# Performance work log

Measured on AMD Instinct MI355X. Metric: run time of the kernel, lower is better.

The kernel has to match this reference:

```python
import jax, jax.numpy as jnp
import numpy as np
import math

B, T, H, W = 32, 256, 16, 16
NE, NH, NL = 768, 12, 8
DH = NE // NH
SEQ_LEN = 1024


def _ln(x, g, b, eps=1e-5):
    m = jnp.mean(x, axis=-1, keepdims=True)
    v = jnp.mean((x - m) ** 2, axis=-1, keepdims=True)
    return (x - m) * jax.lax.rsqrt(v + eps) * g + b


def setup_inputs() -> dict:
    key = jax.random.key(0)
    ks = jax.random.split(key, 24)
    s = 0.02
    d = {}
    d["img_feat"] = jax.random.normal(ks[0], (B, 2048, H, W), jnp.float32)
    d["vm_patches"] = jax.random.normal(ks[1], (B, T, 256), jnp.float32)
    d["fm_patches"] = jax.random.normal(ks[2], (B, T, 256), jnp.float32)
    # token embedding params
    d["conv_w"] = jax.random.normal(ks[3], (NE // 2, 2048, 3, 3), jnp.float32) * s
    d["conv_b"] = jnp.zeros((NE // 2,), jnp.float32)
    d["vm_w"] = jax.random.normal(ks[4], (256, NE // 4), jnp.float32) * s
    d["vm_b"] = jnp.zeros((NE // 4,), jnp.float32)
    d["fm_w"] = jax.random.normal(ks[5], (256, NE // 4), jnp.float32) * s
    d["fm_b"] = jnp.zeros((NE // 4,), jnp.float32)
    d["pos_emb"] = jax.random.normal(ks[6], (SEQ_LEN, NE), jnp.float32) * s
    # stacked per-layer block params (leading dim NL, consumed by lax.scan)
    d["ln1_g"] = jnp.ones((NL, NE), jnp.float32)
    d["ln1_b"] = jnp.zeros((NL, NE), jnp.float32)
    d["Wq"] = jax.random.normal(ks[7], (NL, NE, NE), jnp.float32) * s
    d["bq"] = jnp.zeros((NL, NE), jnp.float32)
    d["Wk"] = jax.random.normal(ks[8], (NL, NE, NE), jnp.float32) * s
    d["bk"] = jnp.zeros((NL, NE), jnp.float32)
    d["Wv"] = jax.random.normal(ks[9], (NL, NE, NE), jnp.float32) * s
    d["bv"] = jnp.zeros((NL, NE), jnp.float32)
    d["Wo"] = jax.random.normal(ks[10], (NL, NE, NE), jnp.float32) * s
    d["bo"] = jnp.zeros((NL, NE), jnp.float32)
    d["ln2_g"] = jnp.ones((NL, NE), jnp.float32)
    d["ln2_b"] = jnp.zeros((NL, NE), jnp.float32)
    d["W1"] = jax.random.normal(ks[11], (NL, NE, 4 * NE), jnp.float32) * s
    d["b1"] = jnp.zeros((NL, 4 * NE), jnp.float32)
    d["W2"] = jax.random.normal(ks[12], (NL, 4 * NE, NE), jnp.float32) * s
    d["b2"] = jnp.zeros((NL, NE), jnp.float32)
    # prediction head params
    d["dec_ln1_g"] = jnp.ones((NE,), jnp.float32)
    d["dec_ln1_b"] = jnp.zeros((NE,), jnp.float32)
    d["dec_w"] = jax.random.normal(ks[13], (NE, NE), jnp.float32) * s
    d["dec_b"] = jnp.zeros((NE,), jnp.float32)
    d["dec_ln2_g"] = jnp.ones((NE,), jnp.float32)
    d["dec_ln2_b"] = jnp.zeros((NE,), jnp.float32)
    d["head_w"] = jax.random.normal(ks[14], (NE, 256), jnp.float32) * s
    d["head_b"] = jnp.zeros((256,), jnp.float32)
    return d


def reference(img_feat, vm_patches, fm_patches, conv_w, conv_b, vm_w, vm_b, fm_w, fm_b,
              pos_emb, ln1_g, ln1_b, Wq, bq, Wk, bk, Wv, bv, Wo, bo, ln2_g, ln2_b,
              W1, b1, W2, b2, dec_ln1_g, dec_ln1_b, dec_w, dec_b, dec_ln2_g, dec_ln2_b,
              head_w, head_b):
    # conv token embed: [B,2048,H,W] -> [B, NE//2, H, W] -> [B, T, NE//2]
    i_emb = jax.lax.conv_general_dilated(
        img_feat, conv_w, (1, 1), "SAME",
        dimension_numbers=("NCHW", "OIHW", "NCHW")) + conv_b[None, :, None, None]
    i_emb = i_emb.reshape(B, NE // 2, T).transpose(0, 2, 1)
    vm_emb = vm_patches @ vm_w + vm_b  # [B,T,NE//4]
    fm_emb = fm_patches @ fm_w + fm_b  # [B,T,NE//4]
    x = jnp.concatenate([i_emb, vm_emb, fm_emb], axis=2) + pos_emb[:T][None]  # [B,T,NE]

    scale = 1.0 / math.sqrt(DH)

    def block(x, p):
        g1, bb1_, wq, bq_, wk, bk_, wv, bv_, wo, bo_, g2, bb2_, w1, bm1, w2, bm2 = p
        h = _ln(x, g1, bb1_)
        q = (h @ wq + bq_).reshape(B, T, NH, DH)
        k = (h @ wk + bk_).reshape(B, T, NH, DH)
        v = (h @ wv + bv_).reshape(B, T, NH, DH)
        # mask in the original forward is hard-coded all-ones -> no masking
        att = jax.nn.softmax(jnp.einsum('bthd,bshd->bhts', q, k) * scale, axis=-1)
        y = jnp.einsum('bhts,bshd->bthd', att, v).reshape(B, T, NE)
        x = x + y @ wo + bo_
        h2 = _ln(x, g2, bb2_)
        x = x + jax.nn.gelu(h2 @ w1 + bm1, approximate=False) @ w2 + bm2
        return x, None

    x, _ = jax.lax.scan(block, x, (ln1_g, ln1_b, Wq, bq, Wk, bk, Wv, bv, Wo, bo,
                                   ln2_g, ln2_b, W1, b1, W2, b2))

    # Transformer_Prediction head
    x = _ln(x, dec_ln1_g, dec_ln1_b)
    x = jax.nn.gelu(x @ dec_w + dec_b, approximate=False)
    x = _ln(x, dec_ln2_g, dec_ln2_b)
    return x @ head_w + head_b  # [B,T,256]
```

## Files before the change

kernel.cpp:

```cpp
#include <hip/hip_runtime.h>
#include <stdint.h>

typedef short short8 __attribute__((ext_vector_type(8)));
typedef float v4f __attribute__((ext_vector_type(4)));

#define EPI_BF16    0
#define EPI_GELU    1
#define EPI_XPOS    3
#define EPI_ATOM    5
#define EPI_ATOMOUT 6

__device__ __forceinline__ uint16_t f2bf(float f) {
  uint32_t u = __float_as_uint(f);
  u += 0x7fffu + ((u >> 16) & 1u);
  return (uint16_t)(u >> 16);
}
__device__ __forceinline__ float bf2f(uint16_t h) {
  return __uint_as_float(((uint32_t)h) << 16);
}
__device__ __forceinline__ float gelu_f(float v) {
  return 0.5f * v * (1.f + erff(v * 0.70710678118654752f));
}
__device__ __forceinline__ void gld16(const uint16_t* g, uint16_t* l) {
  __builtin_amdgcn_global_load_lds(
      (const __attribute__((address_space(1))) void*)g,
      (__attribute__((address_space(3))) void*)l, 16, 0, 0);
}

struct TDesc {
  const float* src;
  uint16_t* dst;
  int K, N, batch;
  long long sstride, dstride;
  int tilesK, tilesN;
  long long tileStart;
};
struct TTable {
  TDesc d[12];
  int nd;
  long long totalTiles;
};

__global__ __launch_bounds__(256) void transpose_convert_kernel(TTable tt) {
  __shared__ float tile[32][33];
  const int tid = threadIdx.x;
  for (long long t = blockIdx.x; t < tt.totalTiles; t += gridDim.x) {
    int di = 0;
    while (di + 1 < tt.nd && t >= tt.d[di + 1].tileStart) di++;
    const TDesc d = tt.d[di];
    long long loc = t - d.tileStart;
    int perB = d.tilesK * d.tilesN;
    int bi = (int)(loc / perB);
    int r = (int)(loc % perB);
    int tk = r / d.tilesN, tn = r % d.tilesN;
    const float* src = d.src + (long long)bi * d.sstride;
    uint16_t* dst = d.dst + (long long)bi * d.dstride;
    int k0 = tk * 32, n0 = tn * 32;
#pragma unroll
    for (int p = 0; p < 4; p++) {
      int i = (tid >> 5) + p * 8;
      int k = k0 + i, n = n0 + (tid & 31);
      float v = 0.f;
      if (k < d.K && n < d.N) v = src[(long long)k * d.N + n];
      tile[i][tid & 31] = v;
    }
    __syncthreads();
#pragma unroll
    for (int p = 0; p < 4; p++) {
      int i = (tid >> 5) + p * 8;
      int n = n0 + i, k = k0 + (tid & 31);
      if (n < d.N && k < d.K) dst[(long long)n * d.K + k] = f2bf(tile[tid & 31][i]);
    }
    __syncthreads();
  }
}

__global__ __launch_bounds__(256) void conv_w_transpose(const float* __restrict__ src,
                                                        uint16_t* __restrict__ dst) {
  __shared__ float lds[2304];
  const int n = blockIdx.y;
  const int c0 = blockIdx.x * 256;
  const float* s = src + (size_t)n * 18432 + (size_t)c0 * 9;
  for (int j = threadIdx.x; j < 2304; j += 256) lds[j] = s[j];
  __syncthreads();
#pragma unroll
  for (int tap = 0; tap < 9; tap++)
    dst[(size_t)n * 18432 + tap * 2048 + c0 + threadIdx.x] =
        f2bf(lds[threadIdx.x * 9 + tap]);
}

__global__ __launch_bounds__(256) void img_pad_kernel(const float* __restrict__ img,
                                                      uint16_t* __restrict__ imgp) {
  __shared__ float tile[64][65];
  const int tid = threadIdx.x;
  const int b = blockIdx.z, ict = blockIdx.y, xyt = blockIdx.x;
  const int ic0 = ict * 64, xy0 = xyt * 64;
  const float* src = img + ((size_t)b * 2048 + ic0) * 256 + xy0;
#pragma unroll
  for (int p = 0; p < 16; p++) {
    int i = (tid >> 6) + p * 4;
    int j = tid & 63;
    tile[i][j] = src[(size_t)i * 256 + j];
  }
  __syncthreads();
#pragma unroll
  for (int p = 0; p < 16; p++) {
    int j = (tid >> 6) + p * 4;
    int i = tid & 63;
    int xy = xy0 + j;
    int y = xy >> 4, x = xy & 15;
    imgp[(((size_t)b * 18 + y + 1) * 18 + (x + 1)) * 2048 + ic0 + i] = f2bf(tile[i][j]);
  }
}

__global__ __launch_bounds__(256) void prep_kernel(const float* __restrict__ bq,
                                                   const float* __restrict__ bk,
                                                   const float* __restrict__ bv,
                                                   float* __restrict__ bqkv,
                                                   const float* __restrict__ vm,
                                                   const float* __restrict__ fm,
                                                   uint16_t* __restrict__ vmb,
                                                   uint16_t* __restrict__ fmb) {
  int idx = blockIdx.x * 256 + threadIdx.x;
  if (idx < 2097152) {
    vmb[idx] = f2bf(vm[idx]);
    fmb[idx] = f2bf(fm[idx]);
  }
  if (idx < 18432) {
    int l = idx / 2304, c = idx % 2304;
    float v = (c < 768) ? bq[l * 768 + c]
                        : ((c < 1536) ? bk[l * 768 + c - 768] : bv[l * 768 + c - 1536]);
    bqkv[idx] = v;
  }
}

__global__ __launch_bounds__(256) void xinit_kernel(const float* __restrict__ convb,
                                                    const float* __restrict__ pos,
                                                    float* __restrict__ x) {
  int idx = blockIdx.x * 256 + threadIdx.x;
  if (idx >= 8192 * 384) return;
  int m = idx / 384, n = idx % 384;
  x[(size_t)m * 768 + n] = convb[n] + pos[(size_t)(m & 255) * 768 + n];
}

template <int BF16IN>
__global__ __launch_bounds__(256) void ln_kernel(const void* __restrict__ inv,
                                                 const float* __restrict__ g,
                                                 const float* __restrict__ bta,
                                                 uint16_t* __restrict__ out) {
  const int row = blockIdx.x;
  const int tid = threadIdx.x;
  const float* inf = (const float*)inv;
  const uint16_t* inb = (const uint16_t*)inv;
  const size_t base = (size_t)row * 768;
  float v[3];
#pragma unroll
  for (int i = 0; i < 3; i++) {
    int c = tid + i * 256;
    v[i] = BF16IN ? bf2f(inb[base + c]) : inf[base + c];
  }
  float s = v[0] + v[1] + v[2];
  float s2 = v[0] * v[0] + v[1] * v[1] + v[2] * v[2];
#pragma unroll
  for (int d = 1; d < 64; d <<= 1) {
    s += __shfl_xor(s, d, 64);
    s2 += __shfl_xor(s2, d, 64);
  }
  __shared__ float ps[4], ps2[4];
  int wave = tid >> 6, lane = tid & 63;
  if (lane == 0) { ps[wave] = s; ps2[wave] = s2; }
  __syncthreads();
  s = ps[0] + ps[1] + ps[2] + ps[3];
  s2 = ps2[0] + ps2[1] + ps2[2] + ps2[3];
  float mean = s * (1.f / 768.f);
  float var = s2 * (1.f / 768.f) - mean * mean;
  float rs = rsqrtf(var + 1e-5f);
#pragma unroll
  for (int i = 0; i < 3; i++) {
    int c = tid + i * 256;
    out[base + c] = f2bf((v[i] - mean) * rs * g[c] + bta[c]);
  }
}

template <int AMODE, int EPI>
__global__ __launch_bounds__(256, 4) void gemm_kernel(
    const uint16_t* __restrict__ A, const uint16_t* __restrict__ Bt,
    const float* __restrict__ bias, int N, int K,
    float* xout,
    const float* __restrict__ pos, int colOff,
    uint16_t* __restrict__ outb, float* __restrict__ outf, int ldc) {
  __shared__ uint16_t ldsA[8192];
  __shared__ uint16_t ldsB[4096];
  const int tid = threadIdx.x;
  const int lane = tid & 63, wave = tid >> 6;
  const int l15 = lane & 15, q8 = (lane >> 4) << 3;
  const int row0 = blockIdx.x * 128, col0 = blockIdx.y * 64;
  const int kPer = K / (int)gridDim.z;
  const int kbeg = kPer * (int)blockIdx.z;
  const int wm = wave & 1, wn = wave >> 1;

  const uint16_t* srcP[6];
  uint16_t* dstP[6];
  bool isA[6];
#pragma unroll
  for (int c = 0; c < 6; c++) {
    int j = wave * 6 + c;
    if (j < 16) {
      int mt8 = j >> 1, ks = j & 1;
      int m = row0 + mt8 * 16 + l15;
      const uint16_t* s;
      if (AMODE == 0) {
        s = A + (size_t)m * K + ks * 32 + q8;
      } else {
        int b_ = m >> 8, y_ = (m >> 4) & 15, x_ = m & 15;
        s = A + ((size_t)((b_ * 18 + y_) * 18 + x_)) * 2048 + ks * 32 + q8;
      }
      srcP[c] = s;
      dstP[c] = &ldsA[j * 512];
      isA[c] = true;
    } else {
      int fb = j - 16;
      int nt = fb >> 1, ks = fb & 1;
      int n = col0 + nt * 16 + l15;
      srcP[c] = Bt + (size_t)n * K + ks * 32 + q8;
      dstP[c] = &ldsB[fb * 512];
      isA[c] = false;
    }
  }

  v4f acc[4][2];
#pragma unroll
  for (int i = 0; i < 4; i++)
#pragma unroll
    for (int j = 0; j < 2; j++) acc[i][j] = (v4f){0.f, 0.f, 0.f, 0.f};

  for (int k0 = kbeg; k0 < kbeg + kPer; k0 += 64) {
    size_t ao;
    if (AMODE == 1) {
      int kq = k0 >> 11;
      int ky = (kq >= 6) ? 2 : ((kq >= 3) ? 1 : 0);
      int kx = kq - ky * 3;
      ao = (size_t)((ky * 18 + kx) * 2048) + (size_t)(k0 & 2047);
    } else {
      ao = (size_t)k0;
    }
    __syncthreads();
#pragma unroll
    for (int c = 0; c < 6; c++) {
      size_t offs = (AMODE == 1) ? (isA[c] ? ao : (size_t)k0) : (size_t)k0;
      gld16(srcP[c] + offs, dstP[c]);
    }
    __syncthreads();
#pragma unroll
    for (int ks = 0; ks < 2; ks++) {
      short8 af[4], bfr[2];
#pragma unroll
      for (int mt = 0; mt < 4; mt++)
        af[mt] = *(const short8*)&ldsA[(((wm * 4 + mt) * 2) + ks) * 512 + lane * 8];
#pragma unroll
      for (int nt = 0; nt < 2; nt++)
        bfr[nt] = *(const short8*)&ldsB[(((wn * 2 + nt) * 2) + ks) * 512 + lane * 8];
#pragma unroll
      for (int mt = 0; mt < 4; mt++)
#pragma unroll
        for (int nt = 0; nt < 2; nt++)
          acc[mt][nt] =
              __builtin_amdgcn_mfma_f32_16x16x32_bf16(af[mt], bfr[nt], acc[mt][nt], 0, 0, 0);
    }
  }

#pragma unroll
  for (int mt = 0; mt < 4; mt++) {
    int mbase = row0 + wm * 64 + mt * 16 + ((lane >> 4) << 2);
#pragma unroll
    for (int nt = 0; nt < 2; nt++) {
      int n = col0 + wn * 32 + nt * 16 + l15;
      float bv;
      if (EPI == EPI_ATOM)
        bv = (bias != nullptr && blockIdx.z == 0) ? bias[n] : 0.f;
      else if (EPI == EPI_ATOMOUT)
        bv = (blockIdx.z == 0) ? bias[n] : 0.f;
      else
        bv = bias[n];
      v4f a = acc[mt][nt];
#pragma unroll
      for (int r = 0; r < 4; r++) {
        int m = mbase + r;
        float v = a[r] + bv;
        if (EPI == EPI_BF16) {
          outb[(size_t)m * ldc + n] = f2bf(v);
        } else if (EPI == EPI_GELU) {
          outb[(size_t)m * ldc + n] = f2bf(gelu_f(v));
        } else if (EPI == EPI_XPOS) {
          xout[(size_t)m * 768 + colOff + n] = v + pos[(size_t)(m & 255) * 768 + colOff + n];
        } else if (EPI == EPI_ATOM) {
          atomicAdd(&xout[(size_t)m * 768 + colOff + n], v);
        } else if (EPI == EPI_ATOMOUT) {
          atomicAdd(&outf[(size_t)m * ldc + n], v);
        }
      }
    }
  }
}

template <int AMODE, int EPI>
__global__ __launch_bounds__(256, 3) void gemm128_kernel(
    const uint16_t* __restrict__ A, const uint16_t* __restrict__ Bt,
    const float* __restrict__ bias, int N, int K,
    float* xout,
    const float* __restrict__ pos, int colOff,
    uint16_t* __restrict__ outb, float* __restrict__ outf, int ldc) {
  __shared__ uint16_t ldsA[8192];
  __shared__ uint16_t ldsB[8192];
  const int tid = threadIdx.x;
  const int lane = tid & 63, wave = tid >> 6;
  const int l15 = lane & 15, q8 = (lane >> 4) << 3;
  const int row0 = blockIdx.x * 128, col0 = blockIdx.y * 128;
  const int kPer = K / (int)gridDim.z;
  const int kbeg = kPer * (int)blockIdx.z;
  const int wm = wave & 1, wn = wave >> 1;

  const uint16_t* srcP[8];
  uint16_t* dstP[8];
  bool isA[8];
#pragma unroll
  for (int c = 0; c < 8; c++) {
    int j = wave * 8 + c;
    if (j < 16) {
      int mt8 = j >> 1, ks = j & 1;
      int m = row0 + mt8 * 16 + l15;
      const uint16_t* s;
      if (AMODE == 0) {
        s = A + (size_t)m * K + ks * 32 + q8;
      } else {
        int b_ = m >> 8, y_ = (m >> 4) & 15, x_ = m & 15;
        s = A + ((size_t)((b_ * 18 + y_) * 18 + x_)) * 2048 + ks * 32 + q8;
      }
      srcP[c] = s;
      dstP[c] = &ldsA[j * 512];
      isA[c] = true;
    } else {
      int fb = j - 16;
      int nt16 = fb >> 1, ks = fb & 1;
      int n = col0 + nt16 * 16 + l15;
      srcP[c] = Bt + (size_t)n * K + ks * 32 + q8;
      dstP[c] = &ldsB[fb * 512];
      isA[c] = false;
    }
  }

  v4f acc[4][4];
#pragma unroll
  for (int i = 0; i < 4; i++)
#pragma unroll
    for (int j = 0; j < 4; j++) acc[i][j] = (v4f){0.f, 0.f, 0.f, 0.f};

  for (int k0 = kbeg; k0 < kbeg + kPer; k0 += 64) {
    size_t ao;
    if (AMODE == 1) {
      int kq = k0 >> 11;
      int ky = (kq >= 6) ? 2 : ((kq >= 3) ? 1 : 0);
      int kx = kq - ky * 3;
      ao = (size_t)((ky * 18 + kx) * 2048) + (size_t)(k0 & 2047);
    } else {
      ao = (size_t)k0;
    }
    __syncthreads();
#pragma unroll
    for (int c = 0; c < 8; c++) {
      size_t offs = (AMODE == 1) ? (isA[c] ? ao : (size_t)k0) : (size_t)k0;
      gld16(srcP[c] + offs, dstP[c]);
    }
    __syncthreads();
#pragma unroll
    for (int ks = 0; ks < 2; ks++) {
      short8 af[4], bfr[4];
#pragma unroll
      for (int mt = 0; mt < 4; mt++)
        af[mt] = *(const short8*)&ldsA[(((wm * 4 + mt) * 2) + ks) * 512 + lane * 8];
#pragma unroll
      for (int nt = 0; nt < 4; nt++)
        bfr[nt] = *(const short8*)&ldsB[(((wn * 4 + nt) * 2) + ks) * 512 + lane * 8];
#pragma unroll
      for (int mt = 0; mt < 4; mt++)
#pragma unroll
        for (int nt = 0; nt < 4; nt++)
          acc[mt][nt] =
              __builtin_amdgcn_mfma_f32_16x16x32_bf16(af[mt], bfr[nt], acc[mt][nt], 0, 0, 0);
    }
  }

#pragma unroll
  for (int mt = 0; mt < 4; mt++) {
    int mbase = row0 + wm * 64 + mt * 16 + ((lane >> 4) << 2);
#pragma unroll
    for (int nt = 0; nt < 4; nt++) {
      int n = col0 + wn * 64 + nt * 16 + l15;
      float bv;
      if (EPI == EPI_ATOM)
        bv = (bias != nullptr && blockIdx.z == 0) ? bias[n] : 0.f;
      else if (EPI == EPI_ATOMOUT)
        bv = (blockIdx.z == 0) ? bias[n] : 0.f;
      else
        bv = bias[n];
      v4f a = acc[mt][nt];
#pragma unroll
      for (int r = 0; r < 4; r++) {
        int m = mbase + r;
        float v = a[r] + bv;
        if (EPI == EPI_BF16) {
          outb[(size_t)m * ldc + n] = f2bf(v);
        } else if (EPI == EPI_GELU) {
          outb[(size_t)m * ldc + n] = f2bf(gelu_f(v));
        } else if (EPI == EPI_XPOS) {
          xout[(size_t)m * 768 + colOff + n] = v + pos[(size_t)(m & 255) * 768 + colOff + n];
        } else if (EPI == EPI_ATOM) {
          atomicAdd(&xout[(size_t)m * 768 + colOff + n], v);
        } else if (EPI == EPI_ATOMOUT) {
          atomicAdd(&outf[(size_t)m * ldc + n], v);
        }
      }
    }
  }
}

__global__ __launch_bounds__(256) void attn_kernel(const uint16_t* __restrict__ qkv,
                                                   uint16_t* __restrict__ y) {
  __shared__ uint16_t KP[18432];
  __shared__ uint16_t Vt[64 * 264];
  uint16_t* Kl = KP;
  uint16_t(*Pl)[16 * 264] = (uint16_t(*)[16 * 264])KP;
  const int tid = threadIdx.x, lane = tid & 63, wave = tid >> 6;
  const int qc = blockIdx.x, h = blockIdx.y, b = blockIdx.z;
  const uint16_t* base = qkv + (size_t)b * 256 * 2304;
  const uint16_t* kb = base + 768 + h * 64;
  const uint16_t* vb = base + 1536 + h * 64;

#pragma unroll
  for (int i = 0; i < 8; i++) {
    int c = i * 256 + tid;
    int t = c >> 3, dh = (c & 7) * 8;
    uint4 d = *(const uint4*)(kb + (size_t)t * 2304 + dh);
    *(uint4*)&Kl[t * 72 + dh] = d;
  }
#pragma unroll
  for (int i = 0; i < 8; i++) {
    int c = i * 256 + tid;
    int t = c >> 3, dh = (c & 7) * 8;
    uint4 d = *(const uint4*)(vb + (size_t)t * 2304 + dh);
    const uint16_t* e = (const uint16_t*)&d;
#pragma unroll
    for (int j = 0; j < 8; j++) Vt[(dh + j) * 264 + t] = e[j];
  }
  __syncthreads();

  const int t0 = qc * 64 + wave * 16;
  const uint16_t* qb = base + h * 64;
  const int l15 = lane & 15, q4 = (lane >> 4) << 3;
  short8 aq0 = *(const short8*)(qb + (size_t)(t0 + l15) * 2304 + q4);
  short8 aq1 = *(const short8*)(qb + (size_t)(t0 + l15) * 2304 + 32 + q4);

  v4f s[16];
#pragma unroll
  for (int jt = 0; jt < 16; jt++) {
    short8 b0 = *(const short8*)&Kl[(jt * 16 + l15) * 72 + q4];
    short8 b1 = *(const short8*)&Kl[(jt * 16 + l15) * 72 + 32 + q4];
    v4f z = (v4f){0.f, 0.f, 0.f, 0.f};
    z = __builtin_amdgcn_mfma_f32_16x16x32_bf16(aq0, b0, z, 0, 0, 0);
    s[jt] = __builtin_amdgcn_mfma_f32_16x16x32_bf16(aq1, b1, z, 0, 0, 0);
  }

  float mx[4], sm[4];
#pragma unroll
  for (int r = 0; r < 4; r++) mx[r] = -1e30f;
#pragma unroll
  for (int jt = 0; jt < 16; jt++)
#pragma unroll
    for (int r = 0; r < 4; r++) {
      float v = s[jt][r] * 0.125f;
      s[jt][r] = v;
      mx[r] = fmaxf(mx[r], v);
    }
#pragma unroll
  for (int r = 0; r < 4; r++) {
#pragma unroll
    for (int d = 1; d < 16; d <<= 1) mx[r] = fmaxf(mx[r], __shfl_xor(mx[r], d, 64));
    sm[r] = 0.f;
  }
#pragma unroll
  for (int jt = 0; jt < 16; jt++)
#pragma unroll
    for (int r = 0; r < 4; r++) {
      float e = __expf(s[jt][r] - mx[r]);
      s[jt][r] = e;
      sm[r] += e;
    }
#pragma unroll
  for (int r = 0; r < 4; r++) {
#pragma unroll
    for (int d = 1; d < 16; d <<= 1) sm[r] += __shfl_xor(sm[r], d, 64);
    sm[r] = 1.f / sm[r];
  }

  __syncthreads();

  const int rbase = (lane >> 4) << 2;
#pragma unroll
  for (int jt = 0; jt < 16; jt++)
#pragma unroll
    for (int r = 0; r < 4; r++)
      Pl[wave][(rbase + r) * 264 + jt * 16 + l15] = f2bf(s[jt][r] * sm[r]);
  __syncthreads();

  v4f o[4];
#pragma unroll
  for (int nt = 0; nt < 4; nt++) o[nt] = (v4f){0.f, 0.f, 0.f, 0.f};
#pragma unroll
  for (int ks = 0; ks < 8; ks++) {
    short8 ap = *(const short8*)&Pl[wave][l15 * 264 + ks * 32 + q4];
#pragma unroll
    for (int nt = 0; nt < 4; nt++) {
      short8 bv8 = *(const short8*)&Vt[(nt * 16 + l15) * 264 + ks * 32 + q4];
      o[nt] = __builtin_amdgcn_mfma_f32_16x16x32_bf16(ap, bv8, o[nt], 0, 0, 0);
    }
  }
#pragma unroll
  for (int nt = 0; nt < 4; nt++)
#pragma unroll
    for (int r = 0; r < 4; r++)
      y[(size_t)(b * 256 + t0 + rbase + r) * 768 + h * 64 + nt * 16 + l15] = f2bf(o[nt][r]);
}

extern "C" void kernel_launch(void* const* d_in, const int* in_sizes, int n_in,
                              void* d_out, int out_size, void* d_ws, size_t ws_size,
                              hipStream_t stream) {
  const float* img   = (const float*)d_in[0];
  const float* vmp   = (const float*)d_in[1];
  const float* fmp   = (const float*)d_in[2];
  const float* convw = (const float*)d_in[3];
  const float* convb = (const float*)d_in[4];
  const float* vmw   = (const float*)d_in[5];
  const float* vmb_  = (const float*)d_in[6];
  const float* fmw   = (const float*)d_in[7];
  const float* fmb_  = (const float*)d_in[8];
  const float* pos   = (const float*)d_in[9];
  const float* ln1g  = (const float*)d_in[10];
  const float* ln1b  = (const float*)d_in[11];
  const float* Wq    = (const float*)d_in[12];
  const float* bq    = (const float*)d_in[13];
  const float* Wk    = (const float*)d_in[14];
  const float* bk    = (const float*)d_in[15];
  const float* Wv    = (const float*)d_in[16];
  const float* bv    = (const float*)d_in[17];
  const float* Wo    = (const float*)d_in[18];
  const float* bo    = (const float*)d_in[19];
  const float* ln2g  = (const float*)d_in[20];
  const float* ln2b  = (const float*)d_in[21];
  const float* W1    = (const float*)d_in[22];
  const float* b1    = (const float*)d_in[23];
  const float* W2    = (const float*)d_in[24];
  const float* b2    = (const float*)d_in[25];
  const float* dln1g = (const float*)d_in[26];
  const float* dln1b = (const float*)d_in[27];
  const float* decw  = (const float*)d_in[28];
  const float* decb  = (const float*)d_in[29];
  const float* dln2g = (const float*)d_in[30];
  const float* dln2b = (const float*)d_in[31];
  const float* headw = (const float*)d_in[32];
  const float* headb = (const float*)d_in[33];
  float* out = (float*)d_out;

  char* wsb = (char*)d_ws;
  size_t off = 0;
  auto alloc = [&](size_t nbytes) -> void* {
    off = (off + 255) & ~(size_t)255;
    void* p = wsb + off;
    off += nbytes;
    return p;
  };
  uint16_t* WtQKV  = (uint16_t*)alloc(8ull * 2304 * 768 * 2);
  uint16_t* WtO    = (uint16_t*)alloc(8ull * 768 * 768 * 2);
  uint16_t* Wt1    = (uint16_t*)alloc(8ull * 3072 * 768 * 2);
  uint16_t* Wt2    = (uint16_t*)alloc(8ull * 768 * 3072 * 2);
  uint16_t* WtConv = (uint16_t*)alloc(384ull * 9 * 2048 * 2);
  uint16_t* WtVm   = (uint16_t*)alloc(192ull * 256 * 2);
  uint16_t* WtFm   = (uint16_t*)alloc(192ull * 256 * 2);
  uint16_t* WtDec  = (uint16_t*)alloc(768ull * 768 * 2);
  uint16_t* WtHead = (uint16_t*)alloc(256ull * 768 * 2);
  uint16_t* imgp   = (uint16_t*)alloc(32ull * 18 * 18 * 2048 * 2);
  uint16_t* vmb    = (uint16_t*)alloc(8192ull * 256 * 2);
  uint16_t* fmb    = (uint16_t*)alloc(8192ull * 256 * 2);
  float*    bqkv   = (float*)alloc(8ull * 2304 * 4);
  float*    x      = (float*)alloc(8192ull * 768 * 4);
  uint16_t* hbuf   = (uint16_t*)alloc(8192ull * 768 * 2);
  uint16_t* qkvb   = (uint16_t*)alloc(8192ull * 2304 * 2);
  uint16_t* ybuf   = (uint16_t*)alloc(8192ull * 768 * 2);
  uint16_t* ubuf   = (uint16_t*)alloc(8192ull * 3072 * 2);
  uint16_t* u2buf  = (uint16_t*)alloc(8192ull * 768 * 2);
  if (off > ws_size) return;

  hipMemsetAsync(imgp, 0, 32ull * 18 * 18 * 2048 * 2, stream);
  hipMemsetAsync(out, 0, (size_t)out_size * 4, stream);

  TTable tt;
  int nd = 0;
  long long tiles = 0;
  auto addT = [&](const float* src, uint16_t* dst, int K, int N, int batch,
                  long long sstr, long long dstr) {
    TDesc& d = tt.d[nd];
    d.src = src; d.dst = dst; d.K = K; d.N = N; d.batch = batch;
    d.sstride = sstr; d.dstride = dstr;
    d.tilesK = (K + 31) / 32; d.tilesN = (N + 31) / 32;
    d.tileStart = tiles;
    tiles += (long long)d.tilesK * d.tilesN * batch;
    nd++;
  };
  addT(Wq, WtQKV,           768, 768, 8, 589824, 1769472);
  addT(Wk, WtQKV + 589824,  768, 768, 8, 589824, 1769472);
  addT(Wv, WtQKV + 1179648, 768, 768, 8, 589824, 1769472);
  addT(Wo, WtO,             768, 768, 8, 589824, 589824);
  addT(W1, Wt1,             768, 3072, 8, 2359296, 2359296);
  addT(W2, Wt2,             3072, 768, 8, 2359296, 2359296);
  addT(vmw, WtVm,           256, 192, 1, 0, 0);
  addT(fmw, WtFm,           256, 192, 1, 0, 0);
  addT(decw, WtDec,         768, 768, 1, 0, 0);
  addT(headw, WtHead,       768, 256, 1, 0, 0);
  tt.nd = nd;
  tt.totalTiles = tiles;

  transpose_convert_kernel<<<(int)tiles, 256, 0, stream>>>(tt);
  conv_w_transpose<<<dim3(8, 384), 256, 0, stream>>>(convw, WtConv);
  img_pad_kernel<<<dim3(4, 32, 32), 256, 0, stream>>>(img, imgp);
  prep_kernel<<<8192, 256, 0, stream>>>(bq, bk, bv, bqkv, vmp, fmp, vmb, fmb);
  xinit_kernel<<<12288, 256, 0, stream>>>(convb, pos, x);

  gemm128_kernel<1, EPI_ATOM><<<dim3(64, 3, 4), 256, 0, stream>>>(
      imgp, WtConv, nullptr, 384, 18432, x, nullptr, 0, nullptr, nullptr, 0);
  gemm_kernel<0, EPI_XPOS><<<dim3(64, 3), 256, 0, stream>>>(
      vmb, WtVm, vmb_, 192, 256, x, pos, 384, nullptr, nullptr, 0);
  gemm_kernel<0, EPI_XPOS><<<dim3(64, 3), 256, 0, stream>>>(
      fmb, WtFm, fmb_, 192, 256, x, pos, 576, nullptr, nullptr, 0);

  for (int l = 0; l < 8; l++) {
    ln_kernel<0><<<8192, 256, 0, stream>>>(x, ln1g + l * 768, ln1b + l * 768, hbuf);
    gemm128_kernel<0, EPI_BF16><<<dim3(64, 18), 256, 0, stream>>>(
        hbuf, WtQKV + (size_t)l * 1769472, bqkv + l * 2304, 2304, 768,
        nullptr, nullptr, 0, qkvb, nullptr, 2304);
    attn_kernel<<<dim3(4, 12, 32), 256, 0, stream>>>(qkvb, ybuf);
    gemm128_kernel<0, EPI_ATOM><<<dim3(64, 6, 2), 256, 0, stream>>>(
        ybuf, WtO + (size_t)l * 589824, bo + l * 768, 768, 768,
        x, nullptr, 0, nullptr, nullptr, 0);
    ln_kernel<0><<<8192, 256, 0, stream>>>(x, ln2g + l * 768, ln2b + l * 768, hbuf);
    gemm128_kernel<0, EPI_GELU><<<dim3(64, 24), 256, 0, stream>>>(
        hbuf, Wt1 + (size_t)l * 2359296, b1 + l * 3072, 3072, 768,
        nullptr, nullptr, 0, ubuf, nullptr, 3072);
    gemm128_kernel<0, EPI_ATOM><<<dim3(64, 6, 2), 256, 0, stream>>>(
        ubuf, Wt2 + (size_t)l * 2359296, b2 + l * 768, 768, 3072,
        x, nullptr, 0, nullptr, nullptr, 0);
  }

  ln_kernel<0><<<8192, 256, 0, stream>>>(x, dln1g, dln1b, hbuf);
  gemm128_kernel<0, EPI_GELU><<<dim3(64, 6), 256, 0, stream>>>(
      hbuf, WtDec, decb, 768, 768, nullptr, nullptr, 0, u2buf, nullptr, 768);
  ln_kernel<1><<<8192, 256, 0, stream>>>(u2buf, dln2g, dln2b, hbuf);
  gemm128_kernel<0, EPI_ATOMOUT><<<dim3(64, 2, 2), 256, 0, stream>>>(
      hbuf, WtHead, headb, 256, 768, nullptr, nullptr, 0, nullptr, out, 256);
}
```

Baseline: 3.629 ms.

## Double-buffer LDS tiles in gemm128 to overlap global loads with MFMA

```diff
diff --git a/kernel.cpp b/kernel.cpp
--- a/kernel.cpp
+++ b/kernel.cpp
@@ -304,25 +304,25 @@
 }
 
 template <int AMODE, int EPI>
-__global__ __launch_bounds__(256, 3) void gemm128_kernel(
+__global__ __launch_bounds__(256, 2) void gemm128_kernel(
     const uint16_t* __restrict__ A, const uint16_t* __restrict__ Bt,
     const float* __restrict__ bias, int N, int K,
     float* xout,
     const float* __restrict__ pos, int colOff,
     uint16_t* __restrict__ outb, float* __restrict__ outf, int ldc) {
-  __shared__ uint16_t ldsA[8192];
-  __shared__ uint16_t ldsB[8192];
+  __shared__ uint16_t lds[2][16384];
   const int tid = threadIdx.x;
   const int lane = tid & 63, wave = tid >> 6;
   const int l15 = lane & 15, q8 = (lane >> 4) << 3;
   const int row0 = blockIdx.x * 128, col0 = blockIdx.y * 128;
   const int kPer = K / (int)gridDim.z;
   const int kbeg = kPer * (int)blockIdx.z;
+  const int nt = kPer >> 6;
   const int wm = wave & 1, wn = wave >> 1;
 
   const uint16_t* srcP[8];
-  uint16_t* dstP[8];
-  bool isA[8];
+  int off[8];
+  bool isAv[8];
 #pragma unroll
   for (int c = 0; c < 8; c++) {
     int j = wave * 8 + c;
@@ -337,65 +337,78 @@
         s = A + ((size_t)((b_ * 18 + y_) * 18 + x_)) * 2048 + ks * 32 + q8;
       }
       srcP[c] = s;
-      dstP[c] = &ldsA[j * 512];
-      isA[c] = true;
+      off[c] = j * 512;
+      isAv[c] = true;
     } else {
       int fb = j - 16;
       int nt16 = fb >> 1, ks = fb & 1;
       int n = col0 + nt16 * 16 + l15;
       srcP[c] = Bt + (size_t)n * K + ks * 32 + q8;
-      dstP[c] = &ldsB[fb * 512];
-      isA[c] = false;
-    }
-  }
-
-  v4f acc[4][4];
-#pragma unroll
-  for (int i = 0; i < 4; i++)
-#pragma unroll
-    for (int j = 0; j < 4; j++) acc[i][j] = (v4f){0.f, 0.f, 0.f, 0.f};
-
-  for (int k0 = kbeg; k0 < kbeg + kPer; k0 += 64) {
-    size_t ao;
+      off[c] = 8192 + fb * 512;
+      isAv[c] = false;
+    }
+  }
+
+  auto STAGE = [&](int t) {
+    int k0 = kbeg + t * 64;
+    size_t aoB = (size_t)k0, aoA;
     if (AMODE == 1) {
       int kq = k0 >> 11;
       int ky = (kq >= 6) ? 2 : ((kq >= 3) ? 1 : 0);
       int kx = kq - ky * 3;
-      ao = (size_t)((ky * 18 + kx) * 2048) + (size_t)(k0 & 2047);
+      aoA = (size_t)((ky * 18 + kx) * 2048) + (size_t)(k0 & 2047);
     } else {
-      ao = (size_t)k0;
-    }
-    __syncthreads();
-#pragma unroll
-    for (int c = 0; c < 8; c++) {
-      size_t offs = (AMODE == 1) ? (isA[c] ? ao : (size_t)k0) : (size_t)k0;
-      gld16(srcP[c] + offs, dstP[c]);
-    }
-    __syncthreads();
+      aoA = aoB;
+    }
+    uint16_t* lb = &lds[t & 1][0];
+#pragma unroll
+    for (int c = 0; c < 8; c++) gld16(srcP[c] + (isAv[c] ? aoA : aoB), lb + off[c]);
+  };
+
+  v4f acc[4][4];
+#pragma unroll
+  for (int i = 0; i < 4; i++)
+#pragma unroll
+    for (int j = 0; j < 4; j++) acc[i][j] = (v4f){0.f, 0.f, 0.f, 0.f};
+
+  STAGE(0);
+  if (nt > 1) STAGE(1);
+
+  for (int t = 0; t < nt; t++) {
+    if (t + 1 < nt)
+      asm volatile("s_waitcnt vmcnt(8)" ::: "memory");
+    else
+      asm volatile("s_waitcnt vmcnt(0)" ::: "memory");
+    __builtin_amdgcn_s_barrier();
+
+    const uint16_t* lb = &lds[t & 1][0];
 #pragma unroll
     for (int ks = 0; ks < 2; ks++) {
       short8 af[4], bfr[4];
 #pragma unroll
       for (int mt = 0; mt < 4; mt++)
-        af[mt] = *(const short8*)&ldsA[(((wm * 4 + mt) * 2) + ks) * 512 + lane * 8];
-#pragma unroll
-      for (int nt = 0; nt < 4; nt++)
-        bfr[nt] = *(const short8*)&ldsB[(((wn * 4 + nt) * 2) + ks) * 512 + lane * 8];
+        af[mt] = *(const short8*)&lb[(((wm * 4 + mt) * 2) + ks) * 512 + lane * 8];
+#pragma unroll
+      for (int nt2 = 0; nt2 < 4; nt2++)
+        bfr[nt2] = *(const short8*)&lb[8192 + (((wn * 4 + nt2) * 2) + ks) * 512 + lane * 8];
 #pragma unroll
       for (int mt = 0; mt < 4; mt++)
 #pragma unroll
-        for (int nt = 0; nt < 4; nt++)
-          acc[mt][nt] =
-              __builtin_amdgcn_mfma_f32_16x16x32_bf16(af[mt], bfr[nt], acc[mt][nt], 0, 0, 0);
-    }
+        for (int nt2 = 0; nt2 < 4; nt2++)
+          acc[mt][nt2] =
+              __builtin_amdgcn_mfma_f32_16x16x32_bf16(af[mt], bfr[nt2], acc[mt][nt2], 0, 0, 0);
+    }
+
+    __builtin_amdgcn_s_barrier();
+    if (t + 2 < nt) STAGE(t + 2);
   }
 
 #pragma unroll
   for (int mt = 0; mt < 4; mt++) {
     int mbase = row0 + wm * 64 + mt * 16 + ((lane >> 4) << 2);
 #pragma unroll
-    for (int nt = 0; nt < 4; nt++) {
-      int n = col0 + wn * 64 + nt * 16 + l15;
+    for (int nt2 = 0; nt2 < 4; nt2++) {
+      int n = col0 + wn * 64 + nt2 * 16 + l15;
       float bv;
       if (EPI == EPI_ATOM)
         bv = (bias != nullptr && blockIdx.z == 0) ? bias[n] : 0.f;
@@ -403,7 +416,7 @@
         bv = (blockIdx.z == 0) ? bias[n] : 0.f;
       else
         bv = bias[n];
-      v4f a = acc[mt][nt];
+      v4f a = acc[mt][nt2];
 #pragma unroll
       for (int r = 0; r < 4; r++) {
         int m = mbase + r;
```

After: 3.521 ms. 1.03x faster.
